# Performance work log

Measured on AMD Instinct MI355X. Metric: run time of the kernel, lower is better.

## Reference

```python
import jax, jax.numpy as jnp
import numpy as np

N = 100000
E = 3200000
G = 64  # number of graphs


def _lin_params(key, fan_in, fan_out):
    k1, k2 = jax.random.split(key)
    bound = 1.0 / np.sqrt(fan_in)
    W = jax.random.uniform(k1, (fan_in, fan_out), jnp.float32, -bound, bound)
    b = jax.random.uniform(k2, (fan_out,), jnp.float32, -bound, bound)
    return W, b


def setup_inputs() -> dict:
    key = jax.random.key(0)
    ks = jax.random.split(key, 12)
    x = jax.random.normal(ks[0], (N, 3), jnp.float32)
    edge_index = jax.random.randint(ks[1], (2, E), 0, N, jnp.int32)
    batch = jnp.sort(jax.random.randint(ks[2], (N,), 0, G, jnp.int32))
    # conv1: in=3, heads=4, out_channels=16, concat=True -> 64
    Wq1, bq1 = _lin_params(ks[3], 3, 64)
    Wk1, bk1 = _lin_params(ks[4], 3, 64)
    Wv1, bv1 = _lin_params(ks[5], 3, 64)
    Ws1, bs1 = _lin_params(ks[6], 3, 64)
    # conv2: in=64, heads=1, out_channels=6, concat=False -> 6
    Wq2, bq2 = _lin_params(ks[7], 64, 6)
    Wk2, bk2 = _lin_params(ks[8], 64, 6)
    Wv2, bv2 = _lin_params(ks[9], 64, 6)
    Ws2, bs2 = _lin_params(ks[10], 64, 6)
    return dict(x=x, edge_index=edge_index, batch=batch,
                Wq1=Wq1, bq1=bq1, Wk1=Wk1, bk1=bk1, Wv1=Wv1, bv1=bv1, Ws1=Ws1, bs1=bs1,
                Wq2=Wq2, bq2=bq2, Wk2=Wk2, bk2=bk2, Wv2=Wv2, bv2=bv2, Ws2=Ws2, bs2=bs2)


def transformer_conv(x, src, dst, Wq, bq, Wk, bk, Wv, bv, Ws, bs, heads, d, concat):
    n = x.shape[0]
    q = (x @ Wq + bq).reshape(n, heads, d)
    k = (x @ Wk + bk).reshape(n, heads, d)
    v = (x @ Wv + bv).reshape(n, heads, d)
    # per-edge attention logits: query at target, key at source  [E, H]
    logits = jnp.einsum('ehd,ehd->eh', q[dst], k[src]) / jnp.sqrt(jnp.float32(d))
    # segment softmax over incoming edges of each target node
    m = jax.ops.segment_max(logits, dst, num_segments=n)          # [N, H]
    a = jnp.exp(logits - m[dst])                                   # [E, H]
    denom = jax.ops.segment_sum(a, dst, num_segments=n)           # [N, H]
    alpha = a / (denom[dst] + 1e-16)
    out = jax.ops.segment_sum(alpha[:, :, None] * v[src], dst, num_segments=n)  # [N,H,d]
    out = out.reshape(n, heads * d) if concat else out.mean(axis=1)
    return out + x @ Ws + bs  # root/skip connection


def reference(x, edge_index, batch,
              Wq1, bq1, Wk1, bk1, Wv1, bv1, Ws1, bs1,
              Wq2, bq2, Wk2, bk2, Wv2, bv2, Ws2, bs2):
    src, dst = edge_index[0], edge_index[1]
    h = transformer_conv(x, src, dst, Wq1, bq1, Wk1, bk1, Wv1, bv1, Ws1, bs1,
                         heads=4, d=16, concat=True)
    h = jax.nn.relu(h)
    # dropout is identity in eval mode
    h = transformer_conv(h, src, dst, Wq2, bq2, Wk2, bk2, Wv2, bv2, Ws2, bs2,
                         heads=1, d=6, concat=False)
    # global mean pool over graphs
    sums = jax.ops.segment_sum(h, batch, num_segments=G)
    cnts = jax.ops.segment_sum(jnp.ones((h.shape[0],), h.dtype), batch, num_segments=G)
    pooled = sums / jnp.maximum(cnts, 1.0)[:, None]
    return jax.nn.log_softmax(pooled, axis=1)
```

## Files before the change

### kernel.cpp

```cpp
#include <hip/hip_runtime.h>
#include <hip/hip_fp16.h>
#include <math.h>

#define N_NODES 100000
#define N_EDGES 3200000
#define N_GRAPHS 64
#define NEG_INF -1e30f

#define NB 196
#define CAP 18432
#define NBLK 512
#define CHUNK 6250

__device__ __forceinline__ void atomAddF(float* p, float v) {
#if defined(__HIP_PLATFORM_AMD__)
    unsafeAtomicAdd(p, v);
#else
    atomicAdd(p, v);
#endif
}

__device__ __forceinline__ float b2f(unsigned w, int sh) {
    return (float)(signed char)(w >> sh);
}

__device__ __forceinline__ float kvdot(const float* q, uint4 w, float* sv_out) {
    float2 s = __half22float2(*(const __half2*)&w.w);
    *sv_out = s.y;
    return s.x * (q[0] * b2f(w.x, 0) + q[1] * b2f(w.x, 8)
                + q[2] * b2f(w.x, 16) + q[3] * b2f(w.x, 24)
                + q[4] * b2f(w.y, 0) + q[5] * b2f(w.y, 8));
}

__global__ void k0_packx(const float* __restrict__ x, float4* __restrict__ xp,
                         uint2* __restrict__ xh) {
    int n = blockIdx.x * 256 + threadIdx.x;
    if (n >= N_NODES) return;
    float x0 = x[3 * n], x1 = x[3 * n + 1], x2 = x[3 * n + 2];
    xp[n] = make_float4(x0, x1, x2, 0.f);
    __half2 h01 = __floats2half2_rn(x0, x1);
    __half2 h2p = __floats2half2_rn(x2, 0.f);
    xh[n] = make_uint2(*(unsigned*)&h01, *(unsigned*)&h2p);
}

__global__ __launch_bounds__(512) void s1_partition(const int* __restrict__ ei,
                                                    int* __restrict__ offs,
                                                    unsigned* __restrict__ pairs) {
    __shared__ unsigned pairbuf[CHUNK];
    __shared__ unsigned sortbuf[CHUNK];
    __shared__ unsigned char buckbuf[CHUNK];
    __shared__ int hist[4][200];
    __shared__ int cur[NB], tmp[NB];
    int tid = threadIdx.x;
    int wp = tid >> 7;
    for (int i = tid; i < 4 * 200; i += 512) ((int*)hist)[i] = 0;
    __syncthreads();
    int gbase = blockIdx.x * CHUNK;
    for (int i = tid; i < CHUNK; i += 512) {
        int src = ei[gbase + i];
        unsigned dst = (unsigned)ei[N_EDGES + gbase + i];
        pairbuf[i] = ((unsigned)src << 9) | (dst & 511u);
        unsigned b = dst >> 9;
        buckbuf[i] = (unsigned char)b;
        atomicAdd(&hist[wp][b], 1);
    }
    __syncthreads();
    if (tid < NB)
        tmp[tid] = hist[0][tid] + hist[1][tid] + hist[2][tid] + hist[3][tid];
    __syncthreads();
    for (int off = 1; off < NB; off <<= 1) {
        int v = 0;
        if (tid < NB && tid >= off) v = tmp[tid - off];
        __syncthreads();
        if (tid < NB) tmp[tid] += v;
        __syncthreads();
    }
    if (tid < NB) {
        int cnt_b = hist[0][tid] + hist[1][tid] + hist[2][tid] + hist[3][tid];
        int excl = tmp[tid] - cnt_b;
        cur[tid] = excl;
        offs[blockIdx.x * NB + tid] = excl;
    }
    __syncthreads();
    for (int i = tid; i < CHUNK; i += 512) {
        int pos = atomicAdd(&cur[buckbuf[i]], 1);
        sortbuf[pos] = pairbuf[i];
    }
    __syncthreads();
    for (int i = tid; i < CHUNK; i += 512)
        pairs[gbase + i] = sortbuf[i];
}

__global__ __launch_bounds__(512) void b4_build(const unsigned* __restrict__ pairs,
                                                const int* __restrict__ offs,
                                                int* __restrict__ rs,
                                                int* __restrict__ re,
                                                int* __restrict__ csr_src) {
    __shared__ int so[NBLK], seg_e[NBLK];
    __shared__ int cnt[512], sc[512], cur[512];
    int b = blockIdx.x;
    int tid = threadIdx.x;
    for (int k = tid; k < NBLK; k += 512) {
        so[k] = offs[k * NB + b];
        seg_e[k] = (b == NB - 1) ? CHUNK : offs[k * NB + b + 1];
    }
    cnt[tid] = 0;
    __syncthreads();
    int wave = tid >> 6, lane = tid & 63;
    for (int k = wave; k < NBLK; k += 8) {
        int s = so[k], e = seg_e[k], gb = k * CHUNK;
        for (int i = s + lane; i < e; i += 64)
            atomicAdd(&cnt[pairs[gb + i] & 511u], 1);
    }
    __syncthreads();
    sc[tid] = cnt[tid];
    __syncthreads();
    for (int off = 1; off < 512; off <<= 1) {
        int v = (tid >= off) ? sc[tid - off] : 0;
        __syncthreads();
        sc[tid] += v;
        __syncthreads();
    }
    int rbase = b * CAP;
    int excl = sc[tid] - cnt[tid];
    cur[tid] = rbase + excl;
    int node = (b << 9) + tid;
    if (node < N_NODES) {
        rs[node] = rbase + excl;
        re[node] = rbase + sc[tid];
    }
    __syncthreads();
    for (int k = wave; k < NBLK; k += 8) {
        int s = so[k], e = seg_e[k], gb = k * CHUNK;
        for (int i = s + lane; i < e; i += 64) {
            unsigned p = pairs[gb + i];
            int pos = atomicAdd(&cur[p & 511u], 1);
            csr_src[pos] = (int)(p >> 9);
        }
    }
}

__global__ void g1_layer1(const float4* __restrict__ xp,
                          const uint2* __restrict__ xh,
                          const float* __restrict__ Wq, const float* __restrict__ bq,
                          const float* __restrict__ Wk, const float* __restrict__ bk,
                          const float* __restrict__ Wv, const float* __restrict__ bv,
                          const float* __restrict__ Ws, const float* __restrict__ bs,
                          const int* __restrict__ rs, const int* __restrict__ re,
                          const int* __restrict__ csr_src,
                          uint2* __restrict__ h1) {
    __shared__ float sWq[192], sWk[192], sWv[192], sWs[192];
    __shared__ float sbq[64], sbk[64], sbv[64], sbs[64];
    for (int i = threadIdx.x; i < 192; i += 256) {
        sWq[i] = Wq[i]; sWk[i] = Wk[i]; sWv[i] = Wv[i]; sWs[i] = Ws[i];
    }
    for (int i = threadIdx.x; i < 64; i += 256) {
        sbq[i] = bq[i]; sbk[i] = bk[i]; sbv[i] = bv[i]; sbs[i] = bs[i];
    }
    __syncthreads();

    int lane = threadIdx.x & 63;
    int u = lane & 15;
    int slot = u >> 2;
    int j0 = u * 4;
    int n = blockIdx.x * 16 + (threadIdx.x >> 6) * 4 + (lane >> 4);

    float4 xc = xp[n];
    float x0 = xc.x, x1 = xc.y, x2 = xc.z;

    float q[4];
#pragma unroll
    for (int i = 0; i < 4; ++i)
        q[i] = 0.25f * (sbq[j0 + i] + x0 * sWq[j0 + i] + x1 * sWq[64 + j0 + i]
                        + x2 * sWq[128 + j0 + i]);
    float t0 = 0.f, t1 = 0.f, t2 = 0.f, tb = 0.f;
#pragma unroll
    for (int i = 0; i < 4; ++i) {
        float qi = q[i];
        t0 += qi * sWk[j0 + i];
        t1 += qi * sWk[64 + j0 + i];
        t2 += qi * sWk[128 + j0 + i];
        tb += qi * sbk[j0 + i];
    }
#pragma unroll
    for (int off = 1; off <= 2; off <<= 1) {
        t0 += __shfl_xor(t0, off);
        t1 += __shfl_xor(t1, off);
        t2 += __shfl_xor(t2, off);
        tb += __shfl_xor(tb, off);
    }
    int tsrc = (lane & 48) | ((lane & 3) << 2) | ((lane >> 2) & 3);
    t0 = __shfl(t0, tsrc, 64);
    t1 = __shfl(t1, tsrc, 64);
    t2 = __shfl(t2, tsrc, 64);
    tb = __shfl(tb, tsrc, 64);

    int row = rs[n];
    int deg = re[n] - row;

    float mA = NEG_INF, dA = 0.f, s0A = 0.f, s1A = 0.f, s2A = 0.f;
    float mB = NEG_INF, dB = 0.f, s0B = 0.f, s1B = 0.f, s2B = 0.f;
    for (int base = 0; base < deg; base += 8) {
        int eA = base + slot, eB = base + 4 + slot;
        bool vA = eA < deg, vB = eB < deg;
        int srcA = vA ? csr_src[row + eA] : 0;
        int srcB = vB ? csr_src[row + eB] : 0;
        uint2 wA = xh[srcA];
        uint2 wB = xh[srcB];
        float2 a01 = __half22float2(*(const __half2*)&wA.x);
        float a2 = __half22float2(*(const __half2*)&wA.y).x;
        float2 b01 = __half22float2(*(const __half2*)&wB.x);
        float b2 = __half22float2(*(const __half2*)&wB.y).x;
        float lA = vA ? (tb + a01.x * t0 + a01.y * t1 + a2 * t2) : NEG_INF;
        float lB = vB ? (tb + b01.x * t0 + b01.y * t1 + b2 * t2) : NEG_INF;
        float mnA = fmaxf(mA, lA);
        float scA = __expf(mA - mnA);
        float aA = vA ? __expf(lA - mnA) : 0.f;
        dA = dA * scA + aA;
        s0A = s0A * scA + aA * a01.x;
        s1A = s1A * scA + aA * a01.y;
        s2A = s2A * scA + aA * a2;
        mA = mnA;
        float mnB = fmaxf(mB, lB);
        float scB = __expf(mB - mnB);
        float aB = vB ? __expf(lB - mnB) : 0.f;
        dB = dB * scB + aB;
        s0B = s0B * scB + aB * b01.x;
        s1B = s1B * scB + aB * b01.y;
        s2B = s2B * scB + aB * b2;
        mB = mnB;
    }
    float m = fmaxf(mA, mB);
    float fA = __expf(mA - m), fB = __expf(mB - m);
    float d = dA * fA + dB * fB;
    float s0 = s0A * fA + s0B * fB;
    float s1 = s1A * fA + s1B * fB;
    float s2 = s2A * fA + s2B * fB;

    float gm = m;
    gm = fmaxf(gm, __shfl_xor(gm, 4));
    gm = fmaxf(gm, __shfl_xor(gm, 8));
    float f = __expf(m - gm);
    d *= f; s0 *= f; s1 *= f; s2 *= f;
#pragma unroll
    for (int off = 4; off <= 8; off <<= 1) {
        d += __shfl_xor(d, off);
        s0 += __shfl_xor(s0, off);
        s1 += __shfl_xor(s1, off);
        s2 += __shfl_xor(s2, off);
    }

    int esrc = (lane & 48) | ((lane >> 2) & 3);
    float dH = __shfl(d, esrc, 64);
    float s0H = __shfl(s0, esrc, 64);
    float s1H = __shfl(s1, esrc, 64);
    float s2H = __shfl(s2, esrc, 64);
    float inv = 1.f / (dH + 1e-16f);
    float fr = dH * inv, r0 = s0H * inv, r1 = s1H * inv, r2 = s2H * inv;

    float o[4];
#pragma unroll
    for (int i = 0; i < 4; ++i) {
        int j = j0 + i;
        float val = fr * sbv[j] + r0 * sWv[j] + r1 * sWv[64 + j] + r2 * sWv[128 + j]
                  + sbs[j] + x0 * sWs[j] + x1 * sWs[64 + j] + x2 * sWs[128 + j];
        o[i] = fmaxf(val, 0.f);
    }
    __half2 p01 = __floats2half2_rn(o[0], o[1]);
    __half2 p23 = __floats2half2_rn(o[2], o[3]);
    h1[(size_t)n * 16 + u] = make_uint2(*(unsigned*)&p01, *(unsigned*)&p23);
}

__global__ void k5_node2(const unsigned* __restrict__ h1,
                         const float* __restrict__ Wq, const float* __restrict__ bq,
                         const float* __restrict__ Wk, const float* __restrict__ bk,
                         const float* __restrict__ Wv, const float* __restrict__ bv,
                         const float* __restrict__ Ws, const float* __restrict__ bs,
                         float* __restrict__ q2, float* __restrict__ s2,
                         uint4* __restrict__ kv2) {
    __shared__ float sWq[384], sWk[384], sWv[384], sWs[384];
    __shared__ float sbq[6], sbk[6], sbv[6], sbs[6];
    for (int i = threadIdx.x; i < 384; i += blockDim.x) {
        sWq[i] = Wq[i]; sWk[i] = Wk[i]; sWv[i] = Wv[i]; sWs[i] = Ws[i];
    }
    if (threadIdx.x < 6) {
        sbq[threadIdx.x] = bq[threadIdx.x];
        sbk[threadIdx.x] = bk[threadIdx.x];
        sbv[threadIdx.x] = bv[threadIdx.x];
        sbs[threadIdx.x] = bs[threadIdx.x];
    }
    __syncthreads();
    int n = blockIdx.x * blockDim.x + threadIdx.x;
    if (n >= N_NODES) return;
    float qa[6], ka[6], va[6], sa[6];
#pragma unroll
    for (int c = 0; c < 6; ++c) { qa[c] = sbq[c]; ka[c] = sbk[c]; va[c] = sbv[c]; sa[c] = sbs[c]; }
    const uint4* hp = reinterpret_cast<const uint4*>(h1 + (size_t)n * 32);
#pragma unroll
    for (int i4 = 0; i4 < 8; ++i4) {
        uint4 hv = hp[i4];
        float2 f01 = __half22float2(*(const __half2*)&hv.x);
        float2 f23 = __half22float2(*(const __half2*)&hv.y);
        float2 f45 = __half22float2(*(const __half2*)&hv.z);
        float2 f67 = __half22float2(*(const __half2*)&hv.w);
        float hvv[8] = {f01.x, f01.y, f23.x, f23.y, f45.x, f45.y, f67.x, f67.y};
#pragma unroll
        for (int uu = 0; uu < 8; ++uu) {
            float hx = hvv[uu];
            int i = i4 * 8 + uu;
#pragma unroll
            for (int c = 0; c < 6; ++c) {
                qa[c] += hx * sWq[i * 6 + c];
                ka[c] += hx * sWk[i * 6 + c];
                va[c] += hx * sWv[i * 6 + c];
                sa[c] += hx * sWs[i * 6 + c];
            }
        }
    }
    const float rsqrt6 = 0.4082482904638631f;
#pragma unroll
    for (int c = 0; c < 6; ++c) {
        q2[(size_t)n * 6 + c] = qa[c] * rsqrt6;
        s2[(size_t)n * 6 + c] = sa[c];
    }
    float mk = 0.f, mv = 0.f;
#pragma unroll
    for (int c = 0; c < 6; ++c) {
        mk = fmaxf(mk, fabsf(ka[c]));
        mv = fmaxf(mv, fabsf(va[c]));
    }
    float sk = fmaxf(mk, 1e-8f) * (1.f / 127.f);
    float sv = fmaxf(mv, 1e-8f) * (1.f / 127.f);
    float isk = 1.f / sk, isv = 1.f / sv;
    int qk[6], qv[6];
#pragma unroll
    for (int c = 0; c < 6; ++c) {
        qk[c] = __float2int_rn(ka[c] * isk);
        qv[c] = __float2int_rn(va[c] * isv);
    }
    uint4 w;
    w.x = (qk[0] & 255) | ((qk[1] & 255) << 8) | ((qk[2] & 255) << 16) | ((qk[3] & 255) << 24);
    w.y = (qk[4] & 255) | ((qk[5] & 255) << 8) | ((qv[0] & 255) << 16) | ((qv[1] & 255) << 24);
    w.z = (qv[2] & 255) | ((qv[3] & 255) << 8) | ((qv[4] & 255) << 16) | ((qv[5] & 255) << 24);
    __half2 hs = __floats2half2_rn(sk, sv);
    w.w = *(unsigned*)&hs;
    kv2[n] = w;
}

__global__ void g2_layer2(const int* __restrict__ rs, const int* __restrict__ re,
                          const int* __restrict__ csr_src,
                          const float* __restrict__ q2,
                          const uint4* __restrict__ kv2,
                          const float* __restrict__ s2,
                          const int* __restrict__ batch,
                          float* __restrict__ psum, float* __restrict__ pcnt) {
    __shared__ float bsum[N_GRAPHS * 6];
    __shared__ float bcnt[N_GRAPHS];
    for (int i = threadIdx.x; i < N_GRAPHS * 6; i += 256) bsum[i] = 0.f;
    for (int i = threadIdx.x; i < N_GRAPHS; i += 256) bcnt[i] = 0.f;
    __syncthreads();

    int node = blockIdx.x * 32 + (threadIdx.x >> 3);
    int lane8 = threadIdx.x & 7;

    float q[6];
#pragma unroll
    for (int c = 0; c < 6; ++c) q[c] = q2[(size_t)node * 6 + c];
    int row = rs[node];
    int deg = re[node] - row;

    float lg[8], svr[8];
    unsigned py[8], pz[8];
#pragma unroll
    for (int i = 0; i < 8; ++i) { lg[i] = NEG_INF; svr[i] = 0.f; py[i] = 0u; pz[i] = 0u; }
    float lmax = NEG_INF;
#pragma unroll
    for (int i = 0; i < 4; ++i) {
        int e = lane8 + i * 8;
        bool v = e < deg;
        int src = v ? csr_src[row + e] : 0;
        uint4 w = kv2[src];
        float svx;
        float l = kvdot(q, w, &svx);
        if (v) {
            lg[i] = l; svr[i] = svx; py[i] = w.y; pz[i] = w.z;
            lmax = fmaxf(lmax, l);
        }
    }
    if (deg > 32) {
#pragma unroll
        for (int i = 4; i < 8; ++i) {
            int e = lane8 + i * 8;
            bool v = e < deg;
            int src = v ? csr_src[row + e] : 0;
            uint4 w = kv2[src];
            float svx;
            float l = kvdot(q, w, &svx);
            if (v) {
                lg[i] = l; svr[i] = svx; py[i] = w.y; pz[i] = w.z;
                lmax = fmaxf(lmax, l);
            }
        }
    }
    float mo = NEG_INF, dov = 0.f;
    float ao[6] = {0.f, 0.f, 0.f, 0.f, 0.f, 0.f};
    for (int e = lane8 + 64; e < deg; e += 8) {
        int src = csr_src[row + e];
        uint4 w = kv2[src];
        float svx;
        float l = kvdot(q, w, &svx);
        float mn = fmaxf(mo, l);
        float scp = __expf(mo - mn);
        float wx = __expf(l - mn);
        float wsx = wx * svx;
        dov = dov * scp + wx;
        ao[0] = ao[0] * scp + wsx * b2f(w.y, 16);
        ao[1] = ao[1] * scp + wsx * b2f(w.y, 24);
        ao[2] = ao[2] * scp + wsx * b2f(w.z, 0);
        ao[3] = ao[3] * scp + wsx * b2f(w.z, 8);
        ao[4] = ao[4] * scp + wsx * b2f(w.z, 16);
        ao[5] = ao[5] * scp + wsx * b2f(w.z, 24);
        mo = mn;
    }
    lmax = fmaxf(lmax, mo);
    lmax = fmaxf(lmax, __shfl_xor(lmax, 1));
    lmax = fmaxf(lmax, __shfl_xor(lmax, 2));
    lmax = fmaxf(lmax, __shfl_xor(lmax, 4));
    if (lmax < -5e29f) lmax = 0.f;

    float d = 0.f;
    float acc[6] = {0.f, 0.f, 0.f, 0.f, 0.f, 0.f};
#pragma unroll
    for (int i = 0; i < 8; ++i) {
        float w = __expf(lg[i] - lmax);
        float ws = w * svr[i];
        d += w;
        acc[0] += ws * b2f(py[i], 16);
        acc[1] += ws * b2f(py[i], 24);
        acc[2] += ws * b2f(pz[i], 0);
        acc[3] += ws * b2f(pz[i], 8);
        acc[4] += ws * b2f(pz[i], 16);
        acc[5] += ws * b2f(pz[i], 24);
    }
    float so = __expf(mo - lmax);
    d += dov * so;
#pragma unroll
    for (int c = 0; c < 6; ++c) acc[c] += ao[c] * so;

#pragma unroll
    for (int off = 1; off <= 4; off <<= 1) {
        d += __shfl_xor(d, off);
#pragma unroll
        for (int c = 0; c < 6; ++c) acc[c] += __shfl_xor(acc[c], off);
    }

    if (lane8 == 0) {
        float inv = 1.f / (d + 1e-16f);
        int g = batch[node];
#pragma unroll
        for (int c = 0; c < 6; ++c) {
            float val = acc[c] * inv + s2[(size_t)node * 6 + c];
            atomicAdd(&bsum[g * 6 + c], val);
        }
        atomicAdd(&bcnt[g], 1.f);
    }
    __syncthreads();
    for (int i = threadIdx.x; i < N_GRAPHS * 6; i += 256) {
        float v = bsum[i];
        if (v != 0.f) atomAddF(psum + i, v);
    }
    for (int i = threadIdx.x; i < N_GRAPHS; i += 256) {
        float v = bcnt[i];
        if (v != 0.f) atomAddF(pcnt + i, v);
    }
}

__global__ void k9_final(const float* __restrict__ psum, const float* __restrict__ pcnt,
                         float* __restrict__ out) {
    int g = threadIdx.x;
    if (g >= N_GRAPHS) return;
    float cnt = fmaxf(pcnt[g], 1.0f);
    float z[6];
    float mx = -1e30f;
#pragma unroll
    for (int c = 0; c < 6; ++c) {
        z[c] = psum[g * 6 + c] / cnt;
        mx = fmaxf(mx, z[c]);
    }
    float se = 0.f;
#pragma unroll
    for (int c = 0; c < 6; ++c) se += __expf(z[c] - mx);
    float lse = mx + logf(se);
#pragma unroll
    for (int c = 0; c < 6; ++c) out[g * 6 + c] = z[c] - lse;
}

extern "C" void kernel_launch(void* const* d_in, const int* in_sizes, int n_in,
                              void* d_out, int out_size, void* d_ws, size_t ws_size,
                              hipStream_t stream) {
    const float* x   = (const float*)d_in[0];
    const int*   ei  = (const int*)d_in[1];
    const int*   bat = (const int*)d_in[2];
    const float* Wq1 = (const float*)d_in[3];  const float* bq1 = (const float*)d_in[4];
    const float* Wk1 = (const float*)d_in[5];  const float* bk1 = (const float*)d_in[6];
    const float* Wv1 = (const float*)d_in[7];  const float* bv1 = (const float*)d_in[8];
    const float* Ws1 = (const float*)d_in[9];  const float* bs1 = (const float*)d_in[10];
    const float* Wq2 = (const float*)d_in[11]; const float* bq2 = (const float*)d_in[12];
    const float* Wk2 = (const float*)d_in[13]; const float* bk2 = (const float*)d_in[14];
    const float* Wv2 = (const float*)d_in[15]; const float* bv2 = (const float*)d_in[16];
    const float* Ws2 = (const float*)d_in[17]; const float* bs2 = (const float*)d_in[18];
    float* out = (float*)d_out;

    char* ws = (char*)d_ws;
    size_t off = 0;
    auto alloc = [&](size_t bytes) -> char* {
        char* p = ws + off;
        off += (bytes + 255) & ~(size_t)255;
        return p;
    };

    float* psum = (float*)alloc((size_t)N_GRAPHS * 6 * 4);
    float* pcnt = (float*)alloc((size_t)N_GRAPHS * 4);
    size_t zero_bytes = off;

    int*      offs    = (int*)     alloc((size_t)NBLK * NB * 4);
    unsigned* pairs   = (unsigned*)alloc((size_t)N_EDGES * 4);
    int*      csr_src = (int*)     alloc((size_t)NB * CAP * 4);
    int*      rsv     = (int*)     alloc((size_t)N_NODES * 4);
    int*      rev     = (int*)     alloc((size_t)N_NODES * 4);
    float4*   xp      = (float4*)  alloc((size_t)N_NODES * 16);
    uint2*    xh      = (uint2*)   alloc((size_t)N_NODES * 8);
    unsigned* h1      = (unsigned*)alloc((size_t)N_NODES * 64 * 2);
    float*    q2      = (float*)   alloc((size_t)N_NODES * 6 * 4);
    float*    s2      = (float*)   alloc((size_t)N_NODES * 6 * 4);
    uint4*    kv2     = (uint4*)   alloc((size_t)N_NODES * 16);

    hipMemsetAsync(d_ws, 0, zero_bytes, stream);

    k0_packx<<<(N_NODES + 255) / 256, 256, 0, stream>>>(x, xp, xh);
    s1_partition<<<NBLK, 512, 0, stream>>>(ei, offs, pairs);
    b4_build<<<NB, 512, 0, stream>>>(pairs, offs, rsv, rev, csr_src);

    g1_layer1<<<N_NODES / 16, 256, 0, stream>>>(xp, xh, Wq1, bq1, Wk1, bk1, Wv1, bv1,
                                                Ws1, bs1, rsv, rev, csr_src,
                                                (uint2*)h1);
    k5_node2<<<(N_NODES + 255) / 256, 256, 0, stream>>>(h1, Wq2, bq2, Wk2, bk2,
                                                        Wv2, bv2, Ws2, bs2,
                                                        q2, s2, kv2);
    g2_layer2<<<N_NODES / 32, 256, 0, stream>>>(rsv, rev, csr_src, q2, kv2, s2,
                                                bat, psum, pcnt);
    k9_final<<<1, 64, 0, stream>>>(psum, pcnt, out);
}
```

Baseline: 163.4 us.

## Stage bucket edges in LDS once and double block size in CSR build

The CSR build kernel now prefix-sums the per-partition segment lengths, copies each bucket's edge pairs from global memory into a compact LDS buffer once, and then runs both the histogram and scatter passes over LDS instead of reading global memory twice. The block size is raised to 1024 threads, and the work loops become flat strided loops over the compacted array. This removes a second global read of the pairs and the load imbalance of short per-segment loops. It adds about 72KB of LDS per block and extra scans and barriers, and it assumes each bucket holds at most CAP edges.

```diff
diff --git a/kernel.cpp b/kernel.cpp
--- a/kernel.cpp
+++ b/kernel.cpp
@@ -91,52 +91,73 @@
         pairs[gbase + i] = sortbuf[i];
 }
 
-__global__ __launch_bounds__(512) void b4_build(const unsigned* __restrict__ pairs,
+#define B4T 1024
+__global__ __launch_bounds__(B4T) void b4_build(const unsigned* __restrict__ pairs,
                                                 const int* __restrict__ offs,
                                                 int* __restrict__ rs,
                                                 int* __restrict__ re,
                                                 int* __restrict__ csr_src) {
-    __shared__ int so[NBLK], seg_e[NBLK];
+    __shared__ unsigned eLDS[CAP];
+    __shared__ int so[NBLK], slen[NBLK], dbase[NBLK];
     __shared__ int cnt[512], sc[512], cur[512];
     int b = blockIdx.x;
     int tid = threadIdx.x;
-    for (int k = tid; k < NBLK; k += 512) {
-        so[k] = offs[k * NB + b];
-        seg_e[k] = (b == NB - 1) ? CHUNK : offs[k * NB + b + 1];
-    }
-    cnt[tid] = 0;
-    __syncthreads();
+
+    for (int k = tid; k < NBLK; k += B4T) {
+        int s = offs[k * NB + b];
+        int e = (b == NB - 1) ? CHUNK : offs[k * NB + b + 1];
+        so[k] = s;
+        slen[k] = e - s;
+    }
+    __syncthreads();
+    if (tid < NBLK) sc[tid] = slen[tid];
+    __syncthreads();
+    for (int off = 1; off < NBLK; off <<= 1) {
+        int v = (tid < NBLK && tid >= off) ? sc[tid - off] : 0;
+        __syncthreads();
+        if (tid < NBLK) sc[tid] += v;
+        __syncthreads();
+    }
+    if (tid < NBLK) dbase[tid] = sc[tid] - slen[tid];
+    __syncthreads();
+    int ne = dbase[NBLK - 1] + slen[NBLK - 1];
+
     int wave = tid >> 6, lane = tid & 63;
-    for (int k = wave; k < NBLK; k += 8) {
-        int s = so[k], e = seg_e[k], gb = k * CHUNK;
-        for (int i = s + lane; i < e; i += 64)
-            atomicAdd(&cnt[pairs[gb + i] & 511u], 1);
-    }
-    __syncthreads();
-    sc[tid] = cnt[tid];
+    for (int k = wave; k < NBLK; k += (B4T / 64)) {
+        int gb = k * CHUNK + so[k];
+        int db = dbase[k], ln = slen[k];
+        for (int i = lane; i < ln; i += 64)
+            eLDS[db + i] = pairs[gb + i];
+    }
+    if (tid < 512) cnt[tid] = 0;
+    __syncthreads();
+
+    for (int i = tid; i < ne; i += B4T)
+        atomicAdd(&cnt[eLDS[i] & 511u], 1);
+    __syncthreads();
+    if (tid < 512) sc[tid] = cnt[tid];
     __syncthreads();
     for (int off = 1; off < 512; off <<= 1) {
-        int v = (tid >= off) ? sc[tid - off] : 0;
+        int v = (tid < 512 && tid >= off) ? sc[tid - off] : 0;
         __syncthreads();
-        sc[tid] += v;
+        if (tid < 512) sc[tid] += v;
         __syncthreads();
     }
     int rbase = b * CAP;
-    int excl = sc[tid] - cnt[tid];
-    cur[tid] = rbase + excl;
-    int node = (b << 9) + tid;
-    if (node < N_NODES) {
-        rs[node] = rbase + excl;
-        re[node] = rbase + sc[tid];
-    }
-    __syncthreads();
-    for (int k = wave; k < NBLK; k += 8) {
-        int s = so[k], e = seg_e[k], gb = k * CHUNK;
-        for (int i = s + lane; i < e; i += 64) {
-            unsigned p = pairs[gb + i];
-            int pos = atomicAdd(&cur[p & 511u], 1);
-            csr_src[pos] = (int)(p >> 9);
+    if (tid < 512) {
+        int excl = sc[tid] - cnt[tid];
+        cur[tid] = rbase + excl;
+        int node = (b << 9) + tid;
+        if (node < N_NODES) {
+            rs[node] = rbase + excl;
+            re[node] = rbase + sc[tid];
         }
+    }
+    __syncthreads();
+    for (int i = tid; i < ne; i += B4T) {
+        unsigned p = eLDS[i];
+        int pos = atomicAdd(&cur[p & 511u], 1);
+        csr_src[pos] = (int)(p >> 9);
     }
 }
 
@@ -539,7 +560,7 @@
 
     k0_packx<<<(N_NODES + 255) / 256, 256, 0, stream>>>(x, xp, xh);
     s1_partition<<<NBLK, 512, 0, stream>>>(ei, offs, pairs);
-    b4_build<<<NB, 512, 0, stream>>>(pairs, offs, rsv, rev, csr_src);
+    b4_build<<<NB, B4T, 0, stream>>>(pairs, offs, rsv, rev, csr_src);
 
     g1_layer1<<<N_NODES / 16, 256, 0, stream>>>(xp, xh, Wq1, bq1, Wk1, bk1, Wv1, bv1,
                                                 Ws1, bs1, rsv, rev, csr_src,
```

After: 144.4 us. 11.7% less time.
